# Optimization experiments

Hardware: AMD Instinct MI355X
Metric: run time of the kernel (lower is better)

## Reference

```python
import jax, jax.numpy as jnp
import numpy as np

WINDOW_SIZE = 11
SIGMA = 1.5
CHANNELS = 3
VAL_RANGE = 2


def _make_window(ws=WINDOW_SIZE, sigma=SIGMA, channel=CHANNELS):
    # gaussian(x) = exp(-(x - ws//2)^2 / (2*sigma^2)), normalized; 2D = outer product
    x = np.arange(ws, dtype=np.float32)
    g = np.exp(-((x - ws // 2) ** 2) / (2.0 * sigma ** 2))
    g = g / g.sum()
    w2d = np.outer(g, g).astype(np.float32)  # (ws, ws)
    # depthwise kernel, OIHW with feature_group_count=channel -> (channel, 1, ws, ws)
    w = np.broadcast_to(w2d[None, None], (channel, 1, ws, ws))
    return jnp.asarray(np.ascontiguousarray(w))


def _dwconv(x, w, channel=CHANNELS):
    # VALID padding, stride 1, depthwise (groups=channel)
    return jax.lax.conv_general_dilated(
        x, w, window_strides=(1, 1), padding='VALID',
        feature_group_count=channel,
        dimension_numbers=('NCHW', 'OIHW', 'NCHW'))


def setup_inputs() -> dict:
    key = jax.random.key(0)
    k1, k2 = jax.random.split(key)
    shape = (16, 3, 512, 512)
    img1 = jax.random.uniform(k1, shape, dtype=jnp.float32)
    img2 = jax.random.uniform(k2, shape, dtype=jnp.float32)
    return {"img1": img1, "img2": img2}


def reference(img1, img2):
    window = _make_window().astype(img1.dtype)
    mu1 = _dwconv(img1, window)
    mu2 = _dwconv(img2, window)
    mu1_sq = mu1 * mu1
    mu2_sq = mu2 * mu2
    mu1_mu2 = mu1 * mu2
    sigma1_sq = _dwconv(img1 * img1, window) - mu1_sq
    sigma2_sq = _dwconv(img2 * img2, window) - mu2_sq
    sigma12 = _dwconv(img1 * img2, window) - mu1_mu2
    C1 = (0.01 * VAL_RANGE) ** 2
    C2 = (0.03 * VAL_RANGE) ** 2
    ssim_map = ((2 * mu1_mu2 + C1) * (2 * sigma12 + C2)) / (
        (mu1_sq + mu2_sq + C1) * (sigma1_sq + sigma2_sq + C2))
    return 1.0 - ssim_map.mean()
```

## Files before the change

kernel.cpp:

```cpp
#include <hip/hip_runtime.h>
#include <math.h>


#define W 512
#define H 512
#define OWID 502
#define NS 16
#define SH 32
#define NPLANES 48
#define NBLOCKS (NPLANES * 2 * NS)
#define NTOTAL 12096192.0

#define G0 0.00102838f
#define G1 0.00759860f
#define G2 0.03600090f
#define G3 0.10936100f
#define G4 0.21300540f
#define G5 0.26601170f

__device__ __constant__ const float Gc[11] = {G0,G1,G2,G3,G4,G5,G4,G3,G2,G1,G0};

#define VTAP(P,D) { \
    constexpr int s_ = (((P) - (D)) % 11 + 11) % 11; \
    constexpr float wv_ = ((D)==0||(D)==10) ? G0 : ((D)==1||(D)==9) ? G1 : \
                          ((D)==2||(D)==8)  ? G2 : ((D)==3||(D)==7) ? G3 : \
                          ((D)==4||(D)==6)  ? G4 : G5; \
    acc1[s_]  = fmaf(wv_, h1,  acc1[s_]); \
    acc2[s_]  = fmaf(wv_, h2,  acc2[s_]); \
    acc11[s_] = fmaf(wv_, h11, acc11[s_]); \
    acc22[s_] = fmaf(wv_, h22, acc22[s_]); \
    acc12[s_] = fmaf(wv_, h12, acc12[s_]); }

#define PHASE(P) { \
    float2* sb_ = sbuf[ir & 1]; \
    sb_[tid] = make_float2(a0, b0); \
    if (tid < 10) sb_[256 + tid] = make_float2(a1, b1); \
    __syncthreads(); \
    { const size_t nro_ = (size_t)min(ir + 1, H - 1) * W; \
      a0 = p1[nro_ + col_main]; b0 = p2[nro_ + col_main]; \
      if (tid < 10) { a1 = p1[nro_ + col_halo]; b1 = p2[nro_ + col_halo]; } } \
    float h1 = 0.f, h2 = 0.f, h11 = 0.f, h22 = 0.f, h12 = 0.f; \
    _Pragma("unroll") \
    for (int k = 0; k < 11; ++k) { \
        float2 v_ = sb_[tid + k]; \
        float wk_ = Gc[k]; \
        float wa_ = wk_ * v_.x, wb_ = wk_ * v_.y; \
        h1 += wa_; h2 += wb_; \
        h11 = fmaf(wa_, v_.x, h11); \
        h22 = fmaf(wb_, v_.y, h22); \
        h12 = fmaf(wa_, v_.y, h12); } \
    VTAP(P,0) VTAP(P,1) VTAP(P,2) VTAP(P,3) VTAP(P,4) VTAP(P,5) \
    VTAP(P,6) VTAP(P,7) VTAP(P,8) VTAP(P,9) VTAP(P,10) \
    { constexpr int cs_ = ((P) + 1) % 11; \
      const int orow_ = ir - 10; \
      if (colok && orow_ >= r0 && orow_ < r1) { \
          float mu1_ = acc1[cs_], mu2_ = acc2[cs_]; \
          float m1s_ = mu1_ * mu1_, m2s_ = mu2_ * mu2_, m12_ = mu1_ * mu2_; \
          float s11_ = acc11[cs_] - m1s_; \
          float s22_ = acc22[cs_] - m2s_; \
          float s12_ = acc12[cs_] - m12_; \
          float num_ = (2.f * m12_ + C1) * (2.f * s12_ + C2); \
          float den_ = (m1s_ + m2s_ + C1) * (s11_ + s22_ + C2); \
          sum += num_ / den_; } \
      acc1[cs_] = 0.f; acc2[cs_] = 0.f; acc11[cs_] = 0.f; \
      acc22[cs_] = 0.f; acc12[cs_] = 0.f; } \
    ++ir; }

__global__ __launch_bounds__(256, 4)
void ssim_main(const float* __restrict__ img1, const float* __restrict__ img2,
               double* __restrict__ partials)
{
    __shared__ float2 sbuf[2][272];
    __shared__ float red[4];

    const int tid   = threadIdx.x;
    const int bid   = blockIdx.x;
    const int half  = bid & 1;
    const int strip = (bid >> 1) % NS;
    const int plane = bid / (2 * NS);

    const int c0 = half * 256;
    const int r0 = strip * SH;
    const int nrows = min(SH, OWID - r0);
    const int r1 = r0 + nrows;
    const int ngroups = (nrows + 20) / 11;

    const size_t pbase = (size_t)plane * (W * H);
    const float* __restrict__ p1 = img1 + pbase;
    const float* __restrict__ p2 = img2 + pbase;

    const int col_main = c0 + tid;
    const int col_halo = min(c0 + 256 + tid, W - 1);
    const bool colok = (c0 + tid) < OWID;

    const float C1 = 4.0e-4f;
    const float C2 = 3.6e-3f;

    float acc1[11], acc2[11], acc11[11], acc22[11], acc12[11];
#pragma unroll
    for (int i = 0; i < 11; ++i) {
        acc1[i] = 0.f; acc2[i] = 0.f; acc11[i] = 0.f; acc22[i] = 0.f; acc12[i] = 0.f;
    }

    float sum = 0.f;
    int ir = r0;

    float a0, b0, a1 = 0.f, b1 = 0.f;
    {
        const size_t ro = (size_t)ir * W;
        a0 = p1[ro + col_main];
        b0 = p2[ro + col_main];
        if (tid < 10) { a1 = p1[ro + col_halo]; b1 = p2[ro + col_halo]; }
    }

    for (int g = 0; g < ngroups; ++g) {
        PHASE(0) PHASE(1) PHASE(2) PHASE(3) PHASE(4) PHASE(5)
        PHASE(6) PHASE(7) PHASE(8) PHASE(9) PHASE(10)
    }

#pragma unroll
    for (int off = 32; off > 0; off >>= 1)
        sum += __shfl_down(sum, off, 64);
    if ((tid & 63) == 0) red[tid >> 6] = sum;
    __syncthreads();
    if (tid == 0)
        partials[bid] = (double)(red[0] + red[1] + red[2] + red[3]);
}

__global__ void ssim_final(const double* __restrict__ partials, float* __restrict__ out)
{
    __shared__ double sd[256];
    const int tid = threadIdx.x;
    double s = 0.0;
    for (int i = tid; i < NBLOCKS; i += 256) s += partials[i];
    sd[tid] = s;
    __syncthreads();
    for (int off = 128; off > 0; off >>= 1) {
        if (tid < off) sd[tid] += sd[tid + off];
        __syncthreads();
    }
    if (tid == 0) out[0] = 1.0f - (float)(sd[0] / NTOTAL);
}

extern "C" void kernel_launch(void* const* d_in, const int* in_sizes, int n_in,
                              void* d_out, int out_size, void* d_ws, size_t ws_size,
                              hipStream_t stream)
{
    const float* img1 = (const float*)d_in[0];
    const float* img2 = (const float*)d_in[1];
    float* out = (float*)d_out;
    double* partials = (double*)d_ws;

    ssim_main<<<NBLOCKS, 256, 0, stream>>>(img1, img2, partials);
    ssim_final<<<1, 256, 0, stream>>>(partials, out);
}
```

Measured before the change: 71.74 us.

## Process two output columns per thread with full-row blocks and float2 loads

Each block now covers a full 512-column row, and each thread computes two adjacent output columns. The horizontal pass reuses 12 shared-memory values across both outputs, and global loads are vectorized to float2, which removes the halo-column reads and half the block count. The rows are split into separate shared arrays, and the final SSIM division is merged into one divide per pixel pair. Doubling the register accumulators lowers the launch bounds occupancy target from 4 to 2, and an ir_end guard is added to skip extra phases.

```diff
diff --git a/kernel.cpp b/kernel.cpp
--- a/kernel.cpp
+++ b/kernel.cpp
@@ -8,7 +8,7 @@
 #define NS 16
 #define SH 32
 #define NPLANES 48
-#define NBLOCKS (NPLANES * 2 * NS)
+#define NBLOCKS (NPLANES * NS)
 #define NTOTAL 12096192.0
 
 #define G0 0.00102838f
@@ -17,100 +17,117 @@
 #define G3 0.10936100f
 #define G4 0.21300540f
 #define G5 0.26601170f
+#define GW(K) (((K)==0||(K)==10) ? G0 : ((K)==1||(K)==9) ? G1 : \
+               ((K)==2||(K)==8)  ? G2 : ((K)==3||(K)==7) ? G3 : \
+               ((K)==4||(K)==6)  ? G4 : G5)
 
-__device__ __constant__ const float Gc[11] = {G0,G1,G2,G3,G4,G5,G4,G3,G2,G1,G0};
+#define HPOS(pp) { \
+    const float a_ = ((pp)&1) ? A[(pp)>>1].y : A[(pp)>>1].x; \
+    const float b_ = ((pp)&1) ? B[(pp)>>1].y : B[(pp)>>1].x; \
+    const float paa_ = a_*a_, pbb_ = b_*b_, pab_ = a_*b_; \
+    if ((pp) < 11) { const float w_ = GW(pp); \
+      h1.x  = fmaf(w_, a_,   h1.x);  h2.x  = fmaf(w_, b_,   h2.x); \
+      h11.x = fmaf(w_, paa_, h11.x); h22.x = fmaf(w_, pbb_, h22.x); \
+      h12.x = fmaf(w_, pab_, h12.x); } \
+    if ((pp) >= 1) { const float w_ = GW((pp)-1); \
+      h1.y  = fmaf(w_, a_,   h1.y);  h2.y  = fmaf(w_, b_,   h2.y); \
+      h11.y = fmaf(w_, paa_, h11.y); h22.y = fmaf(w_, pbb_, h22.y); \
+      h12.y = fmaf(w_, pab_, h12.y); } }
 
 #define VTAP(P,D) { \
     constexpr int s_ = (((P) - (D)) % 11 + 11) % 11; \
-    constexpr float wv_ = ((D)==0||(D)==10) ? G0 : ((D)==1||(D)==9) ? G1 : \
-                          ((D)==2||(D)==8)  ? G2 : ((D)==3||(D)==7) ? G3 : \
-                          ((D)==4||(D)==6)  ? G4 : G5; \
-    acc1[s_]  = fmaf(wv_, h1,  acc1[s_]); \
-    acc2[s_]  = fmaf(wv_, h2,  acc2[s_]); \
-    acc11[s_] = fmaf(wv_, h11, acc11[s_]); \
-    acc22[s_] = fmaf(wv_, h22, acc22[s_]); \
-    acc12[s_] = fmaf(wv_, h12, acc12[s_]); }
+    const float wv_ = GW(D); \
+    acc1[s_].x  = fmaf(wv_, h1.x,  acc1[s_].x);  acc1[s_].y  = fmaf(wv_, h1.y,  acc1[s_].y); \
+    acc2[s_].x  = fmaf(wv_, h2.x,  acc2[s_].x);  acc2[s_].y  = fmaf(wv_, h2.y,  acc2[s_].y); \
+    acc11[s_].x = fmaf(wv_, h11.x, acc11[s_].x); acc11[s_].y = fmaf(wv_, h11.y, acc11[s_].y); \
+    acc22[s_].x = fmaf(wv_, h22.x, acc22[s_].x); acc22[s_].y = fmaf(wv_, h22.y, acc22[s_].y); \
+    acc12[s_].x = fmaf(wv_, h12.x, acc12[s_].x); acc12[s_].y = fmaf(wv_, h12.y, acc12[s_].y); }
 
-#define PHASE(P) { \
-    float2* sb_ = sbuf[ir & 1]; \
-    sb_[tid] = make_float2(a0, b0); \
-    if (tid < 10) sb_[256 + tid] = make_float2(a1, b1); \
+#define SSIMND(MU1,MU2,E11,E22,E12,NN,DD) { \
+    const float m1s_=(MU1)*(MU1), m2s_=(MU2)*(MU2), m12_=(MU1)*(MU2); \
+    const float v11_=(E11)-m1s_, v22_=(E22)-m2s_, v12_=(E12)-m12_; \
+    NN = (2.f*m12_+C1)*(2.f*v12_+C2); \
+    DD = (m1s_+m2s_+C1)*(v11_+v22_+C2); }
+
+#define PHASE(P) if (ir < ir_end) { \
+    const int buf_ = ir & 1; \
+    *(float2*)&s1[buf_][col2] = ra; \
+    *(float2*)&s2[buf_][col2] = rb; \
     __syncthreads(); \
-    { const size_t nro_ = (size_t)min(ir + 1, H - 1) * W; \
-      a0 = p1[nro_ + col_main]; b0 = p2[nro_ + col_main]; \
-      if (tid < 10) { a1 = p1[nro_ + col_halo]; b1 = p2[nro_ + col_halo]; } } \
-    float h1 = 0.f, h2 = 0.f, h11 = 0.f, h22 = 0.f, h12 = 0.f; \
+    { const size_t nro_ = (size_t)min(ir + 1, H - 1) * W + col2; \
+      ra = *(const float2*)(p1 + nro_); rb = *(const float2*)(p2 + nro_); } \
+    float2 A[6], B[6]; \
     _Pragma("unroll") \
-    for (int k = 0; k < 11; ++k) { \
-        float2 v_ = sb_[tid + k]; \
-        float wk_ = Gc[k]; \
-        float wa_ = wk_ * v_.x, wb_ = wk_ * v_.y; \
-        h1 += wa_; h2 += wb_; \
-        h11 = fmaf(wa_, v_.x, h11); \
-        h22 = fmaf(wb_, v_.y, h22); \
-        h12 = fmaf(wa_, v_.y, h12); } \
+    for (int j_ = 0; j_ < 6; ++j_) { \
+        A[j_] = *(const float2*)&s1[buf_][col2 + 2*j_]; \
+        B[j_] = *(const float2*)&s2[buf_][col2 + 2*j_]; } \
+    float2 h1=z2, h2=z2, h11=z2, h22=z2, h12=z2; \
+    HPOS(0) HPOS(1) HPOS(2) HPOS(3) HPOS(4) HPOS(5) \
+    HPOS(6) HPOS(7) HPOS(8) HPOS(9) HPOS(10) HPOS(11) \
     VTAP(P,0) VTAP(P,1) VTAP(P,2) VTAP(P,3) VTAP(P,4) VTAP(P,5) \
     VTAP(P,6) VTAP(P,7) VTAP(P,8) VTAP(P,9) VTAP(P,10) \
     { constexpr int cs_ = ((P) + 1) % 11; \
       const int orow_ = ir - 10; \
-      if (colok && orow_ >= r0 && orow_ < r1) { \
-          float mu1_ = acc1[cs_], mu2_ = acc2[cs_]; \
-          float m1s_ = mu1_ * mu1_, m2s_ = mu2_ * mu2_, m12_ = mu1_ * mu2_; \
-          float s11_ = acc11[cs_] - m1s_; \
-          float s22_ = acc22[cs_] - m2s_; \
-          float s12_ = acc12[cs_] - m12_; \
-          float num_ = (2.f * m12_ + C1) * (2.f * s12_ + C2); \
-          float den_ = (m1s_ + m2s_ + C1) * (s11_ + s22_ + C2); \
-          sum += num_ / den_; } \
-      acc1[cs_] = 0.f; acc2[cs_] = 0.f; acc11[cs_] = 0.f; \
-      acc22[cs_] = 0.f; acc12[cs_] = 0.f; } \
+      if (orow_ >= r0 && orow_ < r1) { \
+        float n0_, d0_, n1_, d1_; \
+        SSIMND(acc1[cs_].x, acc2[cs_].x, acc11[cs_].x, acc22[cs_].x, acc12[cs_].x, n0_, d0_) \
+        SSIMND(acc1[cs_].y, acc2[cs_].y, acc11[cs_].y, acc22[cs_].y, acc12[cs_].y, n1_, d1_) \
+        n0_ = c0ok ? n0_ : 0.f;  d0_ = c0ok ? d0_ : 1.f; \
+        n1_ = c1ok ? n1_ : 0.f;  d1_ = c1ok ? d1_ : 1.f; \
+        sum += fmaf(n0_, d1_, n1_ * d0_) / (d0_ * d1_); } \
+      acc1[cs_]=z2; acc2[cs_]=z2; acc11[cs_]=z2; acc22[cs_]=z2; acc12[cs_]=z2; } \
     ++ir; }
 
-__global__ __launch_bounds__(256, 4)
+__global__ __launch_bounds__(256, 2)
 void ssim_main(const float* __restrict__ img1, const float* __restrict__ img2,
                double* __restrict__ partials)
 {
-    __shared__ float2 sbuf[2][272];
+    __shared__ float s1[2][524];
+    __shared__ float s2[2][524];
     __shared__ float red[4];
 
     const int tid   = threadIdx.x;
     const int bid   = blockIdx.x;
-    const int half  = bid & 1;
-    const int strip = (bid >> 1) % NS;
-    const int plane = bid / (2 * NS);
+    const int strip = bid % NS;
+    const int plane = bid / NS;
 
-    const int c0 = half * 256;
     const int r0 = strip * SH;
     const int nrows = min(SH, OWID - r0);
     const int r1 = r0 + nrows;
+    const int ir_end = r0 + nrows + 10;
     const int ngroups = (nrows + 20) / 11;
 
     const size_t pbase = (size_t)plane * (W * H);
     const float* __restrict__ p1 = img1 + pbase;
     const float* __restrict__ p2 = img2 + pbase;
 
-    const int col_main = c0 + tid;
-    const int col_halo = min(c0 + 256 + tid, W - 1);
-    const bool colok = (c0 + tid) < OWID;
+    const int col2 = 2 * tid;
+    const bool c0ok = (col2)     < OWID;
+    const bool c1ok = (col2 + 1) < OWID;
 
     const float C1 = 4.0e-4f;
     const float C2 = 3.6e-3f;
+    const float2 z2 = make_float2(0.f, 0.f);
 
-    float acc1[11], acc2[11], acc11[11], acc22[11], acc12[11];
+    if (tid < 10) {
+        s1[0][512 + tid] = 0.f; s1[1][512 + tid] = 0.f;
+        s2[0][512 + tid] = 0.f; s2[1][512 + tid] = 0.f;
+    }
+
+    float2 acc1[11], acc2[11], acc11[11], acc22[11], acc12[11];
 #pragma unroll
     for (int i = 0; i < 11; ++i) {
-        acc1[i] = 0.f; acc2[i] = 0.f; acc11[i] = 0.f; acc22[i] = 0.f; acc12[i] = 0.f;
+        acc1[i]=z2; acc2[i]=z2; acc11[i]=z2; acc22[i]=z2; acc12[i]=z2;
     }
 
     float sum = 0.f;
     int ir = r0;
 
-    float a0, b0, a1 = 0.f, b1 = 0.f;
+    float2 ra, rb;
     {
-        const size_t ro = (size_t)ir * W;
-        a0 = p1[ro + col_main];
-        b0 = p2[ro + col_main];
-        if (tid < 10) { a1 = p1[ro + col_halo]; b1 = p2[ro + col_halo]; }
+        const size_t ro = (size_t)ir * W + col2;
+        ra = *(const float2*)(p1 + ro);
+        rb = *(const float2*)(p2 + ro);
     }
 
     for (int g = 0; g < ngroups; ++g) {
```

New measurement: 75.93 us. +5.8%, slower.

## Use single-wavefront blocks to drop barriers and take Gaussian weights as immediates

Applied to the files above, without the earlier changes.

Each block becomes one 64-lane wavefront covering a 64-column chunk and a taller 63-row strip. This lets the per-row __syncthreads be replaced by a compiler memory fence and removes the shared-memory reduction. Gaussian weights are now compile-time immediates instead of constant-memory loads, and the colok check moves into a select. The cost is a larger halo fraction, since each 64-column chunk loads an extra 64 columns, and per-row halo loads that are now unconditional. The code also relies on wavefront-synchronous LDS ordering without an explicit barrier.

```diff
diff --git a/kernel.cpp b/kernel.cpp
--- a/kernel.cpp
+++ b/kernel.cpp
@@ -5,10 +5,11 @@
 #define W 512
 #define H 512
 #define OWID 502
-#define NS 16
-#define SH 32
+#define NS 8
+#define SH 63
+#define NCHUNK 8
 #define NPLANES 48
-#define NBLOCKS (NPLANES * 2 * NS)
+#define NBLOCKS (NPLANES * NCHUNK * NS)
 #define NTOTAL 12096192.0
 
 #define G0 0.00102838f
@@ -17,33 +18,32 @@
 #define G3 0.10936100f
 #define G4 0.21300540f
 #define G5 0.26601170f
-
-__device__ __constant__ const float Gc[11] = {G0,G1,G2,G3,G4,G5,G4,G3,G2,G1,G0};
+#define GW(K) (((K)==0||(K)==10) ? G0 : ((K)==1||(K)==9) ? G1 : \
+               ((K)==2||(K)==8)  ? G2 : ((K)==3||(K)==7) ? G3 : \
+               ((K)==4||(K)==6)  ? G4 : G5)
 
 #define VTAP(P,D) { \
     constexpr int s_ = (((P) - (D)) % 11 + 11) % 11; \
-    constexpr float wv_ = ((D)==0||(D)==10) ? G0 : ((D)==1||(D)==9) ? G1 : \
-                          ((D)==2||(D)==8)  ? G2 : ((D)==3||(D)==7) ? G3 : \
-                          ((D)==4||(D)==6)  ? G4 : G5; \
+    const float wv_ = GW(D); \
     acc1[s_]  = fmaf(wv_, h1,  acc1[s_]); \
     acc2[s_]  = fmaf(wv_, h2,  acc2[s_]); \
     acc11[s_] = fmaf(wv_, h11, acc11[s_]); \
     acc22[s_] = fmaf(wv_, h22, acc22[s_]); \
     acc12[s_] = fmaf(wv_, h12, acc12[s_]); }
 
-#define PHASE(P) { \
+#define PHASE(P) if (ir < ir_end) { \
     float2* sb_ = sbuf[ir & 1]; \
-    sb_[tid] = make_float2(a0, b0); \
-    if (tid < 10) sb_[256 + tid] = make_float2(a1, b1); \
-    __syncthreads(); \
+    sb_[tid]      = make_float2(ra, rb);    \
+    sb_[64 + tid] = make_float2(rc, rd);    \
+    asm volatile("" ::: "memory");          \
     { const size_t nro_ = (size_t)min(ir + 1, H - 1) * W; \
-      a0 = p1[nro_ + col_main]; b0 = p2[nro_ + col_main]; \
-      if (tid < 10) { a1 = p1[nro_ + col_halo]; b1 = p2[nro_ + col_halo]; } } \
+      ra = p1[nro_ + col_main]; rb = p2[nro_ + col_main]; \
+      rc = p1[nro_ + col_halo]; rd = p2[nro_ + col_halo]; } \
     float h1 = 0.f, h2 = 0.f, h11 = 0.f, h22 = 0.f, h12 = 0.f; \
     _Pragma("unroll") \
     for (int k = 0; k < 11; ++k) { \
         float2 v_ = sb_[tid + k]; \
-        float wk_ = Gc[k]; \
+        const float wk_ = GW(k); \
         float wa_ = wk_ * v_.x, wb_ = wk_ * v_.y; \
         h1 += wa_; h2 += wb_; \
         h11 = fmaf(wa_, v_.x, h11); \
@@ -53,7 +53,7 @@
     VTAP(P,6) VTAP(P,7) VTAP(P,8) VTAP(P,9) VTAP(P,10) \
     { constexpr int cs_ = ((P) + 1) % 11; \
       const int orow_ = ir - 10; \
-      if (colok && orow_ >= r0 && orow_ < r1) { \
+      if (orow_ >= r0 && orow_ < r1) { \
           float mu1_ = acc1[cs_], mu2_ = acc2[cs_]; \
           float m1s_ = mu1_ * mu1_, m2s_ = mu2_ * mu2_, m12_ = mu1_ * mu2_; \
           float s11_ = acc11[cs_] - m1s_; \
@@ -61,28 +61,28 @@
           float s12_ = acc12[cs_] - m12_; \
           float num_ = (2.f * m12_ + C1) * (2.f * s12_ + C2); \
           float den_ = (m1s_ + m2s_ + C1) * (s11_ + s22_ + C2); \
-          sum += num_ / den_; } \
+          sum += colok ? (num_ / den_) : 0.f; } \
       acc1[cs_] = 0.f; acc2[cs_] = 0.f; acc11[cs_] = 0.f; \
       acc22[cs_] = 0.f; acc12[cs_] = 0.f; } \
     ++ir; }
 
-__global__ __launch_bounds__(256, 4)
+__global__ __launch_bounds__(64, 4)
 void ssim_main(const float* __restrict__ img1, const float* __restrict__ img2,
                double* __restrict__ partials)
 {
-    __shared__ float2 sbuf[2][272];
-    __shared__ float red[4];
+    __shared__ float2 sbuf[2][128];
 
     const int tid   = threadIdx.x;
     const int bid   = blockIdx.x;
-    const int half  = bid & 1;
-    const int strip = (bid >> 1) % NS;
-    const int plane = bid / (2 * NS);
+    const int chunk = bid % NCHUNK;
+    const int strip = (bid / NCHUNK) % NS;
+    const int plane = bid / (NCHUNK * NS);
 
-    const int c0 = half * 256;
+    const int c0 = chunk * 64;
     const int r0 = strip * SH;
     const int nrows = min(SH, OWID - r0);
     const int r1 = r0 + nrows;
+    const int ir_end = r0 + nrows + 10;
     const int ngroups = (nrows + 20) / 11;
 
     const size_t pbase = (size_t)plane * (W * H);
@@ -90,7 +90,7 @@
     const float* __restrict__ p2 = img2 + pbase;
 
     const int col_main = c0 + tid;
-    const int col_halo = min(c0 + 256 + tid, W - 1);
+    const int col_halo = min(c0 + 64 + tid, W - 1);
     const bool colok = (c0 + tid) < OWID;
 
     const float C1 = 4.0e-4f;
@@ -105,12 +105,11 @@
     float sum = 0.f;
     int ir = r0;
 
-    float a0, b0, a1 = 0.f, b1 = 0.f;
+    float ra, rb, rc, rd;
     {
         const size_t ro = (size_t)ir * W;
-        a0 = p1[ro + col_main];
-        b0 = p2[ro + col_main];
-        if (tid < 10) { a1 = p1[ro + col_halo]; b1 = p2[ro + col_halo]; }
+        ra = p1[ro + col_main]; rb = p2[ro + col_main];
+        rc = p1[ro + col_halo]; rd = p2[ro + col_halo];
     }
 
     for (int g = 0; g < ngroups; ++g) {
@@ -121,10 +120,8 @@
 #pragma unroll
     for (int off = 32; off > 0; off >>= 1)
         sum += __shfl_down(sum, off, 64);
-    if ((tid & 63) == 0) red[tid >> 6] = sum;
-    __syncthreads();
     if (tid == 0)
-        partials[bid] = (double)(red[0] + red[1] + red[2] + red[3]);
+        partials[bid] = (double)sum;
 }
 
 __global__ void ssim_final(const double* __restrict__ partials, float* __restrict__ out)
@@ -151,6 +148,6 @@
     float* out = (float*)d_out;
     double* partials = (double*)d_ws;
 
-    ssim_main<<<NBLOCKS, 256, 0, stream>>>(img1, img2, partials);
+    ssim_main<<<NBLOCKS, 64, 0, stream>>>(img1, img2, partials);
     ssim_final<<<1, 256, 0, stream>>>(partials, out);
 }
```

Result: slower. 77.79 us (+8.4%).
